# Kernel optimization log

Measured on AMD Instinct MI355X. Metric: run time of the kernel, lower is better.

## Reference

```python
import jax, jax.numpy as jnp
import numpy as np
import math

HEADS = 16
SPH = 64      # size_per_head
KEY = 64      # key_size (defaults to size_per_head)
EMB = 1024
STEP = 3


def extract_seq_patches(x, kernel_size, step):
    # x: [B, L, D] -> [B, L, kernel_size, D]; patch j at pos t is x_pad[t - p_left + j*step]
    B, L, D = x.shape
    k_size = kernel_size + (step - 1) * (kernel_size - 1)
    p_right = (k_size - 1) // 2
    p_left = k_size - 1 - p_right
    xp = jnp.pad(x, ((0, 0), (p_left, p_right), (0, 0)))
    xs = [xp[:, i:i + L] for i in range(0, k_size, step)]  # kernel_size slices
    return jnp.stack(xs, axis=2)


def setup_inputs() -> dict:
    key = jax.random.key(0)
    kx, kq, kk, kv = jax.random.split(key, 4)
    B, L = 2, 4096
    x = jax.random.normal(kx, (B, L, EMB), dtype=jnp.float32)
    W_q = jax.random.normal(kq, (EMB, HEADS * KEY), dtype=jnp.float32) * 0.02
    W_k = jax.random.normal(kk, (EMB, HEADS * KEY), dtype=jnp.float32) * 0.02
    W_v = jax.random.normal(kv, (EMB, HEADS * SPH), dtype=jnp.float32) * 0.02
    return {"x": x, "W_q": W_q, "W_k": W_k, "W_v": W_v}


def _forward(x, W_q, W_k, W_v):
    B, L, D = x.shape
    pad_len = STEP - L % STEP
    x = jnp.pad(x, ((0, 0), (0, pad_len), (0, 0)))
    new_len = L + pad_len
    blocks = new_len // STEP
    q = x @ W_q  # [B, new_len, H*KEY]
    k = x @ W_k
    v = x @ W_v
    ksz = 1 + 2 * (STEP - 1)  # kernel_size = 5
    kp = extract_seq_patches(k, ksz, STEP)  # [B, new_len, ksz, H*KEY]
    vp = extract_seq_patches(v, ksz, STEP)
    # reshape to [B, H, step, blocks, d]
    q = q.reshape(B, blocks, STEP, HEADS, KEY).transpose(0, 3, 2, 1, 4)
    kb = k.reshape(B, blocks, STEP, HEADS, KEY).transpose(0, 3, 2, 1, 4)
    vb = v.reshape(B, blocks, STEP, HEADS, SPH).transpose(0, 3, 2, 1, 4)
    # neighbor patches: [B, H, step, blocks, ksz, d]
    kp = kp.reshape(B, blocks, STEP, ksz, HEADS, KEY).transpose(0, 4, 2, 1, 3, 5)
    vp = vp.reshape(B, blocks, STEP, ksz, HEADS, SPH).transpose(0, 4, 2, 1, 3, 5)
    scale = 1.0 / math.sqrt(KEY)
    # strided attention over blocks (same residue mod step): [B,H,step,blocks,blocks]
    a = jnp.einsum('bhsqk,bhspk->bhsqp', q, kb) * scale
    # block-local neighbor attention: [B,H,step,blocks,ksz]
    ap = jnp.einsum('bhsqk,bhsqnk->bhsqn', q, kp) * scale
    A = jax.nn.softmax(jnp.concatenate([a, ap], axis=-1), axis=-1)
    a, ap = A[..., :blocks], A[..., blocks:]
    o = (jnp.einsum('bhsqp,bhspd->bhsqd', a, vb)
         + jnp.einsum('bhsqn,bhsqnd->bhsqd', ap, vp))
    o = o.transpose(0, 3, 2, 1, 4).reshape(B, new_len, HEADS * SPH)
    return o[:, :L]


def reference(x, W_q, W_k, W_v):
    return _forward(x, W_q, W_k, W_v)
```

## Files before the change

### kernel.cpp

```cpp
#include <hip/hip_runtime.h>
#include <hip/hip_bf16.h>

typedef unsigned int u32;
typedef unsigned short u16;
typedef short s8v __attribute__((ext_vector_type(8)));
typedef short s4v __attribute__((ext_vector_type(4)));
typedef float f4v __attribute__((ext_vector_type(4)));
typedef u32 u32x2 __attribute__((ext_vector_type(2)));

#define NBLK 1366
#define VROW 1376
#define QSCALE 0.18033688011112042f

__device__ __forceinline__ u16 f2b(float f) {
  u32 u = __builtin_bit_cast(u32, f);
  u = (u + 0x7FFFu + ((u >> 16) & 1u)) >> 16;
  return (u16)u;
}

__device__ __forceinline__ u32 cvtpk(float a, float b) {
  u32 r;
  asm("v_cvt_pk_bf16_f32 %0, %1, %2" : "=v"(r) : "v"(a), "v"(b));
  return r;
}

__device__ __forceinline__ float fexp2(float x) {
#if defined(__has_builtin)
#if __has_builtin(__builtin_amdgcn_exp2f)
  return __builtin_amdgcn_exp2f(x);
#define FEXP2_DONE 1
#endif
#endif
#ifndef FEXP2_DONE
  float r;
  asm("v_exp_f32 %0, %1" : "=v"(r) : "v"(x));
  return r;
#endif
}

__device__ __forceinline__ void gll16(const void* g, void* l) {
  __builtin_amdgcn_global_load_lds(
      (const __attribute__((address_space(1))) u32*)g,
      (__attribute__((address_space(3))) u32*)l, 16, 0, 0);
}

__device__ __forceinline__ f4v mfma32(s8v a, s8v b, f4v c) {
  return __builtin_amdgcn_mfma_f32_16x16x32_bf16(a, b, c, 0, 0, 0);
}

__device__ __forceinline__ f4v mfma16(s4v a, s4v b, f4v c) {
#if defined(__has_builtin)
#if __has_builtin(__builtin_amdgcn_mfma_f32_16x16x16bf16_1k)
#define MFMA16_BUILTIN 1
#endif
#endif
#ifdef MFMA16_BUILTIN
  return __builtin_amdgcn_mfma_f32_16x16x16bf16_1k(a, b, c, 0, 0, 0);
#else
  f4v d;
  asm("v_mfma_f32_16x16x16_bf16 %0, %1, %2, %3" : "=v"(d) : "v"(a), "v"(b), "v"(c));
  return d;
#endif
}

__global__ __launch_bounds__(256) void k_convert_x(const float* __restrict__ x,
                                                   u16* __restrict__ xb) {
  int gid = blockIdx.x * 256 + threadIdx.x;
  long base = (long)gid * 8;
  if (base >= 8320L * 1024L) return;
  int m = (int)(base >> 10);
  int c = (int)(base & 1023);
  int b = m / 4098;
  int t = m - b * 4098;
  s8v pack;
  if (m < 8196 && t < 4096) {
    const float* src = x + ((size_t)b * 4096 + t) * 1024 + c;
    float4 v0 = *(const float4*)(src);
    float4 v1 = *(const float4*)(src + 4);
    pack[0] = (short)f2b(v0.x); pack[1] = (short)f2b(v0.y);
    pack[2] = (short)f2b(v0.z); pack[3] = (short)f2b(v0.w);
    pack[4] = (short)f2b(v1.x); pack[5] = (short)f2b(v1.y);
    pack[6] = (short)f2b(v1.z); pack[7] = (short)f2b(v1.w);
  } else {
#pragma unroll
    for (int i = 0; i < 8; ++i) pack[i] = 0;
  }
  *(s8v*)(xb + base) = pack;
}

__global__ __launch_bounds__(256) void k_transpose_w(const float* __restrict__ Wq,
                                                     const float* __restrict__ Wk,
                                                     const float* __restrict__ Wv,
                                                     u16* __restrict__ Wt) {
  const float* W = (blockIdx.z == 0) ? Wq : ((blockIdx.z == 1) ? Wk : Wv);
  u16* dst = Wt + (size_t)blockIdx.z * 1024 * 1024;
  __shared__ float tile[32][33];
  int n0 = blockIdx.x * 32, k0 = blockIdx.y * 32;
  int tx = threadIdx.x, ty = threadIdx.y;
#pragma unroll
  for (int i = 0; i < 4; ++i)
    tile[ty + i * 8][tx] = W[(size_t)(k0 + ty + i * 8) * 1024 + n0 + tx];
  __syncthreads();
#pragma unroll
  for (int i = 0; i < 4; ++i)
    dst[(size_t)(n0 + ty + i * 8) * 1024 + k0 + tx] = f2b(tile[tx][ty + i * 8]);
}

__global__ __launch_bounds__(256) void k_gemm_qkv(const u16* __restrict__ xb,
                                                  const u16* __restrict__ Wt,
                                                  u16* __restrict__ Qp,
                                                  u16* __restrict__ Kp,
                                                  u16* __restrict__ Vt) {
  const int wg = blockIdx.x;
  const int sub = wg >> 3;
  const int nz = (wg & 7) * 3 + sub / 65;
  const int mt = sub % 65;
  const int m0 = mt * 128;
  const int n0g = nz * 128;
  const u16* Bg = Wt + (size_t)n0g * 1024;

  __shared__ __align__(16) u16 Al[128 * 64];
  __shared__ __align__(16) u16 Bl[128 * 64];
  const int tid = threadIdx.x;
  const int lane = tid & 63;
  const int w = tid >> 6;
  const int wr = w >> 1, wc = w & 1;
  const int lo = lane & 15, g = lane >> 4;

  f4v acc[4][4];
#pragma unroll
  for (int i = 0; i < 4; ++i)
#pragma unroll
    for (int j = 0; j < 4; ++j) {
      f4v z = {0.f, 0.f, 0.f, 0.f};
      acc[i][j] = z;
    }

  const int lrow = lane >> 3;
  const int schunk = (lane & 7) ^ lrow;

  for (int kt = 0; kt < 1024; kt += 64) {
    __syncthreads();
#pragma unroll
    for (int c = 0; c < 4; ++c) {
      int rloc = w * 32 + c * 8 + lrow;
      gll16(xb + (size_t)(m0 + rloc) * 1024 + kt + schunk * 8, Al + (w * 32 + c * 8) * 64);
      gll16(Bg + (size_t)rloc * 1024 + kt + schunk * 8, Bl + (w * 32 + c * 8) * 64);
    }
    __syncthreads();
#pragma unroll
    for (int ks = 0; ks < 2; ++ks) {
      s8v af[4], bf[4];
#pragma unroll
      for (int i = 0; i < 4; ++i) {
        int ar = wr * 64 + i * 16 + lo;
        af[i] = *(const s8v*)((const char*)Al + ar * 128 + ((ks * 64 + g * 16) ^ ((ar & 7) << 4)));
        int br = wc * 64 + i * 16 + lo;
        bf[i] = *(const s8v*)((const char*)Bl + br * 128 + ((ks * 64 + g * 16) ^ ((br & 7) << 4)));
      }
      __builtin_amdgcn_s_setprio(1);
#pragma unroll
      for (int i = 0; i < 4; ++i)
#pragma unroll
        for (int j = 0; j < 4; ++j)
          acc[i][j] = mfma32(af[i], bf[j], acc[i][j]);
      __builtin_amdgcn_s_setprio(0);
    }
  }

  const int zid = n0g >> 10;
  const float esc = (zid == 0) ? QSCALE : 1.0f;
#pragma unroll
  for (int i = 0; i < 4; ++i) {
#pragma unroll
    for (int r = 0; r < 4; ++r) {
      int m = m0 + wr * 64 + i * 16 + g * 4 + r;
      if (m >= 8196) continue;
      int b = m / 4098;
      int t = m - b * 4098;
      int s = t % 3;
      int p = t / 3;
      int cb = (b * 3 + s) * 16;
#pragma unroll
      for (int j = 0; j < 4; ++j) {
        int n = n0g + wc * 64 + j * 16 + lo;
        int h = (n >> 6) & 15, d = n & 63;
        u16 val = f2b(acc[i][j][r] * esc);
        if (zid == 2) {
          Vt[(size_t)((cb + h) * 64 + d) * VROW + p] = val;
        } else {
          u16* dq = (zid == 0) ? Qp : Kp;
          dq[(size_t)((cb + h) * NBLK + p) * 64 + d] = val;
        }
      }
    }
  }
}

__global__ __launch_bounds__(256) void k_attn(const u16* __restrict__ Qp,
                                              const u16* __restrict__ Kp,
                                              const u16* __restrict__ Vt,
                                              float* __restrict__ out) {
  const int wg = blockIdx.x;
  const int idx = (wg & 7) * 264 + (wg >> 3);
  const int combo = idx / 22;
  const int q0 = (idx % 22) * 64;
  const int b = combo / 48;
  const int rem = combo - b * 48;
  const int s = rem >> 4;
  const int h = rem & 15;
  const int tid = threadIdx.x, lane = tid & 63, w = tid >> 6;
  const int lo = lane & 15, g = lane >> 4;

  const u16* Qg = Qp + (size_t)combo * (NBLK * 64);
  const u16* Kg = Kp + (size_t)combo * (NBLK * 64);
  const u16* Vg = Vt + (size_t)combo * (64 * VROW);

  __shared__ __align__(16) u16 Kl[64 * 64];
  __shared__ __align__(16) u16 Vl[64 * 64];

  const int pq_e = q0 + w * 16 + lo;
  const int qc = (pq_e < NBLK) ? pq_e : (NBLK - 1);
  s8v qf0 = *(const s8v*)(Qg + (size_t)qc * 64 + g * 8);
  s8v qf1 = *(const s8v*)(Qg + (size_t)qc * 64 + 32 + g * 8);

  s4v onesf;
  onesf[0] = onesf[1] = onesf[2] = onesf[3] = (short)0x3F80;

  f4v oacc[4];
#pragma unroll
  for (int i = 0; i < 4; ++i) {
    f4v z = {0.f, 0.f, 0.f, 0.f};
    oacc[i] = z;
  }
  f4v den_acc = {0.f, 0.f, 0.f, 0.f};

  const int lrow = lane >> 3;
  const int schunk = (lane & 7) ^ lrow;

  for (int j0 = 0; j0 < NBLK; j0 += 64) {
    __syncthreads();
#pragma unroll
    for (int c = 0; c < 2; ++c) {
      int rloc = w * 16 + c * 8 + lrow;
      gll16(Kg + (size_t)(j0 + rloc) * 64 + schunk * 8, Kl + (w * 16 + c * 8) * 64);
      gll16(Vg + (size_t)rloc * VROW + j0 + schunk * 8, Vl + (w * 16 + c * 8) * 64);
    }
    __syncthreads();

    f4v sacc[4];
    __builtin_amdgcn_s_setprio(1);
#pragma unroll
    for (int kb = 0; kb < 4; ++kb) {
      f4v z = {0.f, 0.f, 0.f, 0.f};
      int row = kb * 16 + lo;
      int sw = (row & 7) << 4;
      s8v kf0 = *(const s8v*)((const char*)Kl + row * 128 + ((g * 16) ^ sw));
      s8v kf1 = *(const s8v*)((const char*)Kl + row * 128 + ((64 + g * 16) ^ sw));
      z = mfma32(kf0, qf0, z);
      sacc[kb] = mfma32(kf1, qf1, z);
    }
    __builtin_amdgcn_s_setprio(0);

    s4v ef[4];
    const bool special = (j0 >= q0 - 64 && j0 <= q0 + 64) || (j0 + 64 > NBLK);
    if (special) {
#pragma unroll
      for (int kb = 0; kb < 4; ++kb) {
        float e[4];
#pragma unroll
        for (int r = 0; r < 4; ++r) {
          int j = j0 + kb * 16 + g * 4 + r;
          float ev = fexp2(sacc[kb][r]);
          int dd = j - pq_e;
          float fac = (j < NBLK) ? (((dd <= 2) && (dd >= -2)) ? 2.f : 1.f) : 0.f;
          e[r] = ev * fac;
        }
        u32x2 w2;
        w2[0] = cvtpk(e[0], e[1]);
        w2[1] = cvtpk(e[2], e[3]);
        ef[kb] = __builtin_bit_cast(s4v, w2);
      }
    } else {
#pragma unroll
      for (int kb = 0; kb < 4; ++kb) {
        u32x2 w2;
        w2[0] = cvtpk(fexp2(sacc[kb][0]), fexp2(sacc[kb][1]));
        w2[1] = cvtpk(fexp2(sacc[kb][2]), fexp2(sacc[kb][3]));
        ef[kb] = __builtin_bit_cast(s4v, w2);
      }
    }

    __builtin_amdgcn_s_setprio(1);
#pragma unroll
    for (int kb = 0; kb < 4; ++kb)
      den_acc = mfma16(ef[kb], onesf, den_acc);
#pragma unroll
    for (int db = 0; db < 4; ++db) {
      int row = db * 16 + lo;
      int sw = (row & 7) << 4;
#pragma unroll
      for (int kb = 0; kb < 4; ++kb) {
        s4v vf = *(const s4v*)((const char*)Vl + row * 128 + ((kb * 32 + g * 8) ^ sw));
        oacc[db] = mfma16(ef[kb], vf, oacc[db]);
      }
    }
    __builtin_amdgcn_s_setprio(0);
  }

  const int hbase = h * 64;
#pragma unroll
  for (int r = 0; r < 4; ++r) {
    int pq = q0 + w * 16 + g * 4 + r;
    float dden = den_acc[r];
    dden += (pq == 0 || pq == NBLK - 1) ? 2.f : ((pq == 1 || pq == NBLK - 2) ? 1.f : 0.f);
    float rr = 1.f / dden;
    int t = 3 * pq + s;
    if (pq < NBLK && t < 4096) {
      float* orow = out + ((size_t)b * 4096 + t) * 1024 + hbase;
#pragma unroll
      for (int db = 0; db < 4; ++db)
        orow[db * 16 + lo] = oacc[db][r] * rr;
    }
  }
}

extern "C" void kernel_launch(void* const* d_in, const int* in_sizes, int n_in,
                              void* d_out, int out_size, void* d_ws, size_t ws_size,
                              hipStream_t stream) {
  const float* x  = (const float*)d_in[0];
  const float* Wq = (const float*)d_in[1];
  const float* Wk = (const float*)d_in[2];
  const float* Wv = (const float*)d_in[3];
  float* out = (float*)d_out;

  u16* ws = (u16*)d_ws;
  u16* xb = ws;
  u16* Wt = xb + 8519680;
  u16* Qp = Wt + 3145728;
  u16* Kp = Qp + 8392704;
  u16* Vt = Kp + 8392704;

  k_convert_x<<<4160, 256, 0, stream>>>(x, xb);
  k_transpose_w<<<dim3(32, 32, 3), dim3(32, 8), 0, stream>>>(Wq, Wk, Wv, Wt);
  hipMemsetAsync(Vt, 0, (size_t)(8454144 + 256) * sizeof(u16), stream);
  k_gemm_qkv<<<dim3(1560), 256, 0, stream>>>(xb, Wt, Qp, Kp, Vt);
  k_attn<<<dim3(2112), 256, 0, stream>>>(Qp, Kp, Vt, out);
}
```

Measured before the change: 249.9 us.

## Rewrite QKV GEMM with 256x256 tiles and a 4-stage async LDS pipeline

Replaces the 128x128 QKV GEMM tile, which staged 64-wide K slices with two full barriers per step, with 256x256 tiles on 512 threads. K is consumed in 32-wide slices through a 4-buffer LDS ring filled by direct global-to-LDS loads issued three stages ahead, with a waitcnt on outstanding memory ops before each barrier. Blocks are remapped so each XCD gets a contiguous range of tiles, aiming for better L2 reuse. The larger tile and 128 accumulator registers per lane raise register and LDS pressure, and there are fewer workgroups overall (396), which may leave CUs underused.

```diff
diff --git a/kernel.cpp b/kernel.cpp
--- a/kernel.cpp
+++ b/kernel.cpp
@@ -106,75 +106,104 @@
     dst[(size_t)(n0 + ty + i * 8) * 1024 + k0 + tx] = f2b(tile[tx][ty + i * 8]);
 }
 
-__global__ __launch_bounds__(256) void k_gemm_qkv(const u16* __restrict__ xb,
-                                                  const u16* __restrict__ Wt,
-                                                  u16* __restrict__ Qp,
-                                                  u16* __restrict__ Kp,
-                                                  u16* __restrict__ Vt) {
-  const int wg = blockIdx.x;
-  const int sub = wg >> 3;
-  const int nz = (wg & 7) * 3 + sub / 65;
-  const int mt = sub % 65;
-  const int m0 = mt * 128;
-  const int n0g = nz * 128;
+__global__ __launch_bounds__(512, 2) void k_gemm_qkv(const u16* __restrict__ xb,
+                                                     const u16* __restrict__ Wt,
+                                                     u16* __restrict__ Qp,
+                                                     u16* __restrict__ Kp,
+                                                     u16* __restrict__ Vt) {
+  const int orig = blockIdx.x;
+  const int xcd = orig & 7, sub = orig >> 3;
+  const int wgid = (xcd < 4 ? xcd * 50 : 4 * 50 + (xcd - 4) * 49) + sub;
+  const int nz = wgid / 33, mt = wgid % 33;
+  const int m0 = mt * 256;
+  const int n0g = nz * 256;
   const u16* Bg = Wt + (size_t)n0g * 1024;
 
-  __shared__ __align__(16) u16 Al[128 * 64];
-  __shared__ __align__(16) u16 Bl[128 * 64];
+  __shared__ __align__(16) u16 lds[4 * 16384];
+
   const int tid = threadIdx.x;
   const int lane = tid & 63;
   const int w = tid >> 6;
-  const int wr = w >> 1, wc = w & 1;
+  const int wm = w >> 2, wn = w & 3;
   const int lo = lane & 15, g = lane >> 4;
 
-  f4v acc[4][4];
-#pragma unroll
-  for (int i = 0; i < 4; ++i)
+  const int csrc = (lane & 3) ^ ((lane >> 3) & 3);
+  const int lrow = lane >> 2;
+  const bool isA = (w < 4);
+  const int w3 = w & 3;
+  const int rsw = (g ^ ((lo >> 1) & 3)) << 4;
+
+  f4v acc[8][4];
+#pragma unroll
+  for (int i = 0; i < 8; ++i)
 #pragma unroll
     for (int j = 0; j < 4; ++j) {
       f4v z = {0.f, 0.f, 0.f, 0.f};
       acc[i][j] = z;
     }
 
-  const int lrow = lane >> 3;
-  const int schunk = (lane & 7) ^ lrow;
-
-  for (int kt = 0; kt < 1024; kt += 64) {
-    __syncthreads();
-#pragma unroll
-    for (int c = 0; c < 4; ++c) {
-      int rloc = w * 32 + c * 8 + lrow;
-      gll16(xb + (size_t)(m0 + rloc) * 1024 + kt + schunk * 8, Al + (w * 32 + c * 8) * 64);
-      gll16(Bg + (size_t)rloc * 1024 + kt + schunk * 8, Bl + (w * 32 + c * 8) * 64);
-    }
-    __syncthreads();
-#pragma unroll
-    for (int ks = 0; ks < 2; ++ks) {
-      s8v af[4], bf[4];
-#pragma unroll
-      for (int i = 0; i < 4; ++i) {
-        int ar = wr * 64 + i * 16 + lo;
-        af[i] = *(const s8v*)((const char*)Al + ar * 128 + ((ks * 64 + g * 16) ^ ((ar & 7) << 4)));
-        int br = wc * 64 + i * 16 + lo;
-        bf[i] = *(const s8v*)((const char*)Bl + br * 128 + ((ks * 64 + g * 16) ^ ((br & 7) << 4)));
-      }
-      __builtin_amdgcn_s_setprio(1);
-#pragma unroll
-      for (int i = 0; i < 4; ++i)
-#pragma unroll
-        for (int j = 0; j < 4; ++j)
-          acc[i][j] = mfma32(af[i], bf[j], acc[i][j]);
-      __builtin_amdgcn_s_setprio(0);
-    }
-  }
+  const u16* gsrc0 = isA ? (xb + (size_t)(m0 + w3 * 64 + lrow) * 1024)
+                         : (Bg + (size_t)(w3 * 64 + lrow) * 1024);
+
+#define STAGE(nn)                                                            \
+  {                                                                          \
+    const int sn_ = (nn);                                                    \
+    const int kt2_ = sn_ * 32;                                               \
+    u16* sb2_ = lds + (sn_ & 3) * 16384 + (isA ? 0 : 8192) + w3 * 2048;      \
+    _Pragma("unroll")                                                        \
+    for (int q = 0; q < 4; ++q) {                                            \
+      gll16(gsrc0 + (size_t)q * 16 * 1024 + kt2_ + csrc * 8, sb2_ + q * 512);\
+    }                                                                        \
+  }
+
+#define GPERIOD(nn, DOSTAGE, VMLIT)                                          \
+  {                                                                          \
+    const int n_ = (nn);                                                     \
+    if (DOSTAGE) { STAGE(n_ + 3); }                                          \
+    asm volatile("s_waitcnt vmcnt(" VMLIT ")" ::: "memory");                 \
+    __builtin_amdgcn_s_barrier();                                            \
+    asm volatile("" ::: "memory");                                           \
+    const char* sA_ = (const char*)(lds + (n_ & 3) * 16384);                 \
+    const char* sB_ = sA_ + 16384;                                           \
+    s8v af_[8];                                                              \
+    s8v bf_[4];                                                              \
+    _Pragma("unroll")                                                        \
+    for (int i = 0; i < 8; ++i)                                              \
+      af_[i] = *(const s8v*)(sA_ + (wm * 128 + i * 16 + lo) * 64 + rsw);     \
+    _Pragma("unroll")                                                        \
+    for (int j = 0; j < 4; ++j)                                              \
+      bf_[j] = *(const s8v*)(sB_ + (wn * 64 + j * 16 + lo) * 64 + rsw);      \
+    __builtin_amdgcn_s_setprio(1);                                           \
+    _Pragma("unroll")                                                        \
+    for (int i = 0; i < 8; ++i)                                              \
+      _Pragma("unroll")                                                      \
+      for (int j = 0; j < 4; ++j)                                            \
+        acc[i][j] = mfma32(af_[i], bf_[j], acc[i][j]);                       \
+    __builtin_amdgcn_s_setprio(0);                                           \
+    asm volatile("s_waitcnt lgkmcnt(0)" ::: "memory");                       \
+    __builtin_amdgcn_s_barrier();                                            \
+    asm volatile("" ::: "memory");                                           \
+  }
+
+  STAGE(0);
+  STAGE(1);
+  STAGE(2);
+
+  for (int n = 0; n < 29; ++n) GPERIOD(n, true, "12");
+  GPERIOD(29, false, "8");
+  GPERIOD(30, false, "4");
+  GPERIOD(31, false, "0");
+
+#undef GPERIOD
+#undef STAGE
 
   const int zid = n0g >> 10;
   const float esc = (zid == 0) ? QSCALE : 1.0f;
 #pragma unroll
-  for (int i = 0; i < 4; ++i) {
+  for (int i = 0; i < 8; ++i) {
 #pragma unroll
     for (int r = 0; r < 4; ++r) {
-      int m = m0 + wr * 64 + i * 16 + g * 4 + r;
+      int m = m0 + wm * 128 + i * 16 + g * 4 + r;
       if (m >= 8196) continue;
       int b = m / 4098;
       int t = m - b * 4098;
@@ -183,7 +212,7 @@
       int cb = (b * 3 + s) * 16;
 #pragma unroll
       for (int j = 0; j < 4; ++j) {
-        int n = n0g + wc * 64 + j * 16 + lo;
+        int n = n0g + wn * 64 + j * 16 + lo;
         int h = (n >> 6) & 15, d = n & 63;
         u16 val = f2b(acc[i][j][r] * esc);
         if (zid == 2) {
@@ -344,6 +373,6 @@
   k_convert_x<<<4160, 256, 0, stream>>>(x, xb);
   k_transpose_w<<<dim3(32, 32, 3), dim3(32, 8), 0, stream>>>(Wq, Wk, Wv, Wt);
   hipMemsetAsync(Vt, 0, (size_t)(8454144 + 256) * sizeof(u16), stream);
-  k_gemm_qkv<<<dim3(1560), 256, 0, stream>>>(xb, Wt, Qp, Kp, Vt);
+  k_gemm_qkv<<<dim3(396), 512, 0, stream>>>(xb, Wt, Qp, Kp, Vt);
   k_attn<<<dim3(2112), 256, 0, stream>>>(Qp, Kp, Vt, out);
 }
```

Result: slower. 384.8 us (+54.0%).

## Double-buffer QKV GEMM K-loop and stage V transpose through LDS

Applied to the files above, without the earlier changes.

The QKV projection GEMM now uses two 32-wide K stages in LDS, so loading the next chunk overlaps MFMA work on the current one, replacing the single-buffer load/sync/compute loop. The V epilogue writes the tile to shared memory first and then emits strided per-row stores into the transposed V layout, replacing scattered per-element stores. The grid changes from a swizzled 1D index to a plain 3D (m, n, z) launch, which drops the XCD-aware block ordering. In exchange, each K step has half the work per sync, there are more barriers, and the V store loop is serial per thread.

```diff
diff --git a/kernel.cpp b/kernel.cpp
--- a/kernel.cpp
+++ b/kernel.cpp
@@ -111,22 +111,27 @@
                                                   u16* __restrict__ Qp,
                                                   u16* __restrict__ Kp,
                                                   u16* __restrict__ Vt) {
-  const int wg = blockIdx.x;
-  const int sub = wg >> 3;
-  const int nz = (wg & 7) * 3 + sub / 65;
-  const int mt = sub % 65;
-  const int m0 = mt * 128;
-  const int n0g = nz * 128;
-  const u16* Bg = Wt + (size_t)n0g * 1024;
-
-  __shared__ __align__(16) u16 Al[128 * 64];
-  __shared__ __align__(16) u16 Bl[128 * 64];
+  const int zid = blockIdx.z;
+  const int m0 = blockIdx.x * 128;
+  const int n0 = blockIdx.y * 128;
+  const u16* Bg = Wt + (size_t)zid * 1024 * 1024 + (size_t)n0 * 1024;
+
+  __shared__ __align__(16) u16 shl[16384];
+  u16* A0 = shl;
+  u16* A1 = shl + 4096;
+  u16* B0 = shl + 8192;
+  u16* B1 = shl + 12288;
+
   const int tid = threadIdx.x;
   const int lane = tid & 63;
   const int w = tid >> 6;
   const int wr = w >> 1, wc = w & 1;
   const int lo = lane & 15, g = lane >> 4;
 
+  const int lrow = lane >> 2;
+  const int csrc = (lane & 3) ^ ((lane >> 3) & 3);
+  const int rsw = (g ^ ((lo >> 1) & 3)) << 4;
+
   f4v acc[4][4];
 #pragma unroll
   for (int i = 0; i < 4; ++i)
@@ -136,62 +141,99 @@
       acc[i][j] = z;
     }
 
-  const int lrow = lane >> 3;
-  const int schunk = (lane & 7) ^ lrow;
-
-  for (int kt = 0; kt < 1024; kt += 64) {
-    __syncthreads();
-#pragma unroll
-    for (int c = 0; c < 4; ++c) {
-      int rloc = w * 32 + c * 8 + lrow;
-      gll16(xb + (size_t)(m0 + rloc) * 1024 + kt + schunk * 8, Al + (w * 32 + c * 8) * 64);
-      gll16(Bg + (size_t)rloc * 1024 + kt + schunk * 8, Bl + (w * 32 + c * 8) * 64);
-    }
-    __syncthreads();
-#pragma unroll
-    for (int ks = 0; ks < 2; ++ks) {
-      s8v af[4], bf[4];
-#pragma unroll
-      for (int i = 0; i < 4; ++i) {
-        int ar = wr * 64 + i * 16 + lo;
-        af[i] = *(const s8v*)((const char*)Al + ar * 128 + ((ks * 64 + g * 16) ^ ((ar & 7) << 4)));
-        int br = wc * 64 + i * 16 + lo;
-        bf[i] = *(const s8v*)((const char*)Bl + br * 128 + ((ks * 64 + g * 16) ^ ((br & 7) << 4)));
-      }
-      __builtin_amdgcn_s_setprio(1);
-#pragma unroll
-      for (int i = 0; i < 4; ++i)
-#pragma unroll
-        for (int j = 0; j < 4; ++j)
-          acc[i][j] = mfma32(af[i], bf[j], acc[i][j]);
-      __builtin_amdgcn_s_setprio(0);
-    }
-  }
-
-  const int zid = n0g >> 10;
+  auto stage = [&](int kt, u16* Ab, u16* Bb) {
+#pragma unroll
+    for (int c = 0; c < 2; ++c) {
+      int rloc = w * 32 + c * 16 + lrow;
+      gll16(xb + (size_t)(m0 + rloc) * 1024 + kt + csrc * 8,
+            Ab + (w * 32 + c * 16) * 32);
+      gll16(Bg + (size_t)rloc * 1024 + kt + csrc * 8,
+            Bb + (w * 32 + c * 16) * 32);
+    }
+  };
+
+  auto compute = [&](const u16* Ab, const u16* Bb) {
+    s8v af[4], bf[4];
+#pragma unroll
+    for (int i = 0; i < 4; ++i) {
+      int ar = wr * 64 + i * 16 + lo;
+      af[i] = *(const s8v*)((const char*)Ab + ar * 64 + rsw);
+      int br = wc * 64 + i * 16 + lo;
+      bf[i] = *(const s8v*)((const char*)Bb + br * 64 + rsw);
+    }
+#pragma unroll
+    for (int i = 0; i < 4; ++i)
+#pragma unroll
+      for (int j = 0; j < 4; ++j)
+        acc[i][j] = mfma32(af[i], bf[j], acc[i][j]);
+  };
+
+  stage(0, A0, B0);
+  __syncthreads();
+#pragma unroll 1
+  for (int kk = 0; kk < 16; ++kk) {
+    int kt = kk * 2 * 32;
+    stage(kt + 32, A1, B1);
+    compute(A0, B0);
+    __syncthreads();
+    if (kk < 15) stage(kt + 64, A0, B0);
+    compute(A1, B1);
+    __syncthreads();
+  }
+
   const float esc = (zid == 0) ? QSCALE : 1.0f;
-#pragma unroll
-  for (int i = 0; i < 4; ++i) {
-#pragma unroll
-    for (int r = 0; r < 4; ++r) {
-      int m = m0 + wr * 64 + i * 16 + g * 4 + r;
-      if (m >= 8196) continue;
-      int b = m / 4098;
-      int t = m - b * 4098;
-      int s = t % 3;
-      int p = t / 3;
-      int cb = (b * 3 + s) * 16;
-#pragma unroll
-      for (int j = 0; j < 4; ++j) {
-        int n = n0g + wc * 64 + j * 16 + lo;
-        int h = (n >> 6) & 15, d = n & 63;
-        u16 val = f2b(acc[i][j][r] * esc);
-        if (zid == 2) {
-          Vt[(size_t)((cb + h) * 64 + d) * VROW + p] = val;
-        } else {
-          u16* dq = (zid == 0) ? Qp : Kp;
-          dq[(size_t)((cb + h) * NBLK + p) * 64 + d] = val;
+  if (zid != 2) {
+    u16* dq = (zid == 0) ? Qp : Kp;
+#pragma unroll
+    for (int i = 0; i < 4; ++i) {
+#pragma unroll
+      for (int r = 0; r < 4; ++r) {
+        int m = m0 + wr * 64 + i * 16 + g * 4 + r;
+        if (m >= 8196) continue;
+        int b = m / 4098;
+        int t = m - b * 4098;
+        int s = t % 3;
+        int p = t / 3;
+        int cb = (b * 3 + s) * 16;
+#pragma unroll
+        for (int j = 0; j < 4; ++j) {
+          int n = n0 + wc * 64 + j * 16 + lo;
+          int h = n >> 6, d = n & 63;
+          dq[(size_t)((cb + h) * NBLK + p) * 64 + d] = f2b(acc[i][j][r] * esc);
         }
+      }
+    }
+  } else {
+    u16* tile = shl;
+#pragma unroll
+    for (int i = 0; i < 4; ++i)
+#pragma unroll
+      for (int r = 0; r < 4; ++r) {
+        int ml = wr * 64 + i * 16 + g * 4 + r;
+#pragma unroll
+        for (int j = 0; j < 4; ++j) {
+          int nl = wc * 64 + j * 16 + lo;
+          tile[ml * 128 + nl] = f2b(acc[i][j][r]);
+        }
+      }
+    __syncthreads();
+    for (int pair = tid; pair < 384; pair += 256) {
+      int nl = pair & 127;
+      int s = pair >> 7;
+      int n = n0 + nl;
+      int h = n >> 6, d = n & 63;
+      for (int b = 0; b < 2; ++b) {
+        int mlo = m0 > b * 4098 ? m0 : b * 4098;
+        int cap = b * 4098 + 4096;
+        int mhi = (m0 + 128 < cap) ? m0 + 128 : cap;
+        if (mlo >= mhi) continue;
+        int t_lo = mlo - b * 4098;
+        int add = (s - (t_lo % 3) + 3) % 3;
+        int t = t_lo + add;
+        int tend = mhi - b * 4098;
+        u16* dst = Vt + (size_t)(((b * 3 + s) * 16 + h) * 64 + d) * VROW;
+        for (; t < tend; t += 3)
+          dst[t / 3] = tile[(b * 4098 + t - m0) * 128 + nl];
       }
     }
   }
@@ -344,6 +386,6 @@
   k_convert_x<<<4160, 256, 0, stream>>>(x, xb);
   k_transpose_w<<<dim3(32, 32, 3), dim3(32, 8), 0, stream>>>(Wq, Wk, Wv, Wt);
   hipMemsetAsync(Vt, 0, (size_t)(8454144 + 256) * sizeof(u16), stream);
-  k_gemm_qkv<<<dim3(1560), 256, 0, stream>>>(xb, Wt, Qp, Kp, Vt);
+  k_gemm_qkv<<<dim3(65, 8, 3), 256, 0, stream>>>(xb, Wt, Qp, Kp, Vt);
   k_attn<<<dim3(2112), 256, 0, stream>>>(Qp, Kp, Vt, out);
 }
```

Result: faster. 222.5 us (-11.0%).
